# Kernel tuning notes

Hardware: AMD Instinct MI355X
Metric: run time of the kernel (lower is better)

## Reference

```python
import jax, jax.numpy as jnp
import numpy as np

ND, NA, E, EL, H, F = 100000, 50000, 500000, 200000, 128, 128


def setup_inputs() -> dict:
    key = jax.random.key(0)
    ks = jax.random.split(key, 20)
    def W(k, shape):
        return jax.random.normal(k, shape, dtype=jnp.float32) * 0.05
    inp = {
        'doc_x': jax.random.normal(ks[0], (ND, F), dtype=jnp.float32),
        'author_node_id': jnp.arange(NA, dtype=jnp.int64 if jax.config.jax_enable_x64 else jnp.int32),
        'edge_index': jnp.stack([
            jax.random.randint(ks[1], (E,), 0, ND),   # doc src
            jax.random.randint(ks[2], (E,), 0, NA),   # author dst
        ]),
        'edge_label_index': jnp.stack([
            jax.random.randint(ks[3], (EL,), 0, ND),
            jax.random.randint(ks[4], (EL,), 0, NA),
        ]),
        'doc_lin_W': W(ks[5], (F, H)), 'doc_lin_b': W(ks[6], (H,)),
        'author_emb': W(ks[7], (NA, H)),
        'c1_da_Wl': W(ks[8], (H, H)), 'c1_da_bl': W(ks[9], (H,)), 'c1_da_Wr': W(ks[10], (H, H)),
        'c1_ad_Wl': W(ks[11], (H, H)), 'c1_ad_bl': W(ks[12], (H,)), 'c1_ad_Wr': W(ks[13], (H, H)),
        'c2_da_Wl': W(ks[14], (H, H)), 'c2_da_bl': W(ks[15], (H,)), 'c2_da_Wr': W(ks[16], (H, H)),
        'c2_ad_Wl': W(ks[17], (H, H)), 'c2_ad_bl': W(ks[18], (H,)), 'c2_ad_Wr': W(ks[19], (H, H)),
    }
    return inp


def sage(x_src, x_dst, src, dst, num_dst, Wl, bl, Wr):
    # PyG SAGEConv (aggr='mean'): lin_l(mean_j x_src[j]) + lin_r(x_dst)
    msg = x_src[src]                                            # [E, H]
    agg = jax.ops.segment_sum(msg, dst, num_segments=num_dst)   # [num_dst, H]
    deg = jax.ops.segment_sum(jnp.ones_like(dst, dtype=x_src.dtype), dst, num_segments=num_dst)
    agg = agg / jnp.maximum(deg, 1.0)[:, None]
    return agg @ Wl + bl + x_dst @ Wr


def reference(doc_x, author_node_id, edge_index, edge_label_index,
              doc_lin_W, doc_lin_b, author_emb,
              c1_da_Wl, c1_da_bl, c1_da_Wr, c1_ad_Wl, c1_ad_bl, c1_ad_Wr,
              c2_da_Wl, c2_da_bl, c2_da_Wr, c2_ad_Wl, c2_ad_bl, c2_ad_Wr):
    x_doc = doc_x @ doc_lin_W + doc_lin_b          # [ND, H]
    x_author = author_emb[author_node_id]          # [NA, H]
    src_d, dst_a = edge_index[0], edge_index[1]
    # layer 1 (per-edge-type convs, to_hetero semantics) + ReLU
    h_a = sage(x_doc, x_author, src_d, dst_a, NA, c1_da_Wl, c1_da_bl, c1_da_Wr)
    h_d = sage(x_author, x_doc, dst_a, src_d, ND, c1_ad_Wl, c1_ad_bl, c1_ad_Wr)
    h_a, h_d = jax.nn.relu(h_a), jax.nn.relu(h_d)
    # layer 2
    o_a = sage(h_d, h_a, src_d, dst_a, NA, c2_da_Wl, c2_da_bl, c2_da_Wr)
    o_d = sage(h_a, h_d, dst_a, src_d, ND, c2_ad_Wl, c2_ad_bl, c2_ad_Wr)
    # edge scorer: dot product of gathered endpoint embeddings
    pred = (o_d[edge_label_index[0]] * o_a[edge_label_index[1]]).sum(-1)  # [EL]
    return pred
```

## Files before the change

### kernel.cpp

```cpp
#include <hip/hip_runtime.h>

typedef unsigned short u16;
typedef __attribute__((ext_vector_type(8))) short vbf16x8;
typedef __attribute__((ext_vector_type(4))) float vf32x4;

__device__ __forceinline__ float bf2f(u16 u) {
    union { unsigned int i; float f; } v; v.i = ((unsigned int)u) << 16; return v.f;
}
__device__ __forceinline__ u16 f2bf(float f) {
    union { float f; unsigned int i; } v; v.f = f;
    return (u16)((v.i + 0x7fffu + ((v.i >> 16) & 1u)) >> 16);
}

struct TPack { const float* src[9]; u16* dst[9]; };

#define NBUK 256
#define NBLK_BIN 256
#define SCAP 24
#define OVFCAP 32768
#define PACK_SH 17

__global__ __launch_bounds__(256) void mega_prep_bin(
    TPack p, const float* __restrict__ emb, const int* __restrict__ ids,
    u16* __restrict__ xauth, int NA,
    const int* __restrict__ src, const int* __restrict__ dst,
    unsigned* __restrict__ stageD, unsigned* __restrict__ stageA,
    int* __restrict__ cntD, int* __restrict__ cntA,
    uint2* __restrict__ ovfD, uint2* __restrict__ ovfA, int* __restrict__ ovfn,
    int E, int shD, int shA, int prepB) {
    int b = blockIdx.x;
    if (b >= prepB) {
        __shared__ int lcnt[NBUK];
        int bb = b - prepB;
        const bool isD = bb < NBLK_BIN;
        const int blk = isD ? bb : bb - NBLK_BIN;
        const int* key = isD ? src : dst;
        const int* val = isD ? dst : src;
        const int shift = isD ? shD : shA;
        unsigned* stage = isD ? stageD : stageA;
        int* cnt = isD ? cntD : cntA;
        uint2* ovf = isD ? ovfD : ovfA;
        int* on = ovfn + (isD ? 0 : 1);
        const int per = (E + NBLK_BIN - 1) / NBLK_BIN;
        const int beg = blk * per;
        const int end = min(beg + per, E);
        for (int i = threadIdx.x; i < NBUK; i += 256) lcnt[i] = 0;
        __syncthreads();
        for (int e = beg + (int)threadIdx.x; e < end; e += 256) {
            int k = key[e], v = val[e];
            int bkt = k >> shift;
            int slot = atomicAdd(&lcnt[bkt], 1);
            if (slot < SCAP) {
                unsigned local = (unsigned)(k - (bkt << shift));
                stage[((size_t)bkt * NBLK_BIN + blk) * SCAP + slot] =
                    (local << PACK_SH) | (unsigned)v;
            } else {
                int oi = atomicAdd(on, 1);
                if (oi < OVFCAP) ovf[oi] = make_uint2((unsigned)k, (unsigned)v);
            }
        }
        __syncthreads();
        for (int i = threadIdx.x; i < NBUK; i += 256)
            cnt[(size_t)i * NBLK_BIN + blk] = min(lcnt[i], SCAP);
        return;
    }
    if (b < 576) {
        int mat = b / 64;
        const float* s = p.src[mat];
        u16* d = p.dst[mat];
        int i = (b % 64) * 256 + threadIdx.x;
        int k = i >> 7, n = i & 127;
        d[(size_t)n * 128 + k] = f2bf(s[(size_t)k * 128 + n]);
    } else {
        int gid = (b - 576) * 256 + threadIdx.x;
        if (gid >= NA * 16) return;
        int n = gid >> 4, f = gid & 15;
        int id = ids[n];
        const float* s = emb + (size_t)id * 128 + f * 8;
        float4 lo = *(const float4*)(s);
        float4 hi = *(const float4*)(s + 4);
        u16 o[8] = {f2bf(lo.x), f2bf(lo.y), f2bf(lo.z), f2bf(lo.w),
                    f2bf(hi.x), f2bf(hi.y), f2bf(hi.z), f2bf(hi.w)};
        *(uint4*)(xauth + (size_t)n * 128 + f * 8) = *(const uint4*)o;
    }
}

__global__ __launch_bounds__(256) void bucket_count(
    const unsigned* __restrict__ stageD, const unsigned* __restrict__ stageA,
    const int* __restrict__ cntD, const int* __restrict__ cntA,
    const uint2* __restrict__ ovfD, const uint2* __restrict__ ovfA,
    const int* __restrict__ ovfn,
    int* __restrict__ cnt_d, int* __restrict__ cnt_a,
    int ND, int NA, int shD, int shA) {
    __shared__ int hist[1024];
    __shared__ int segc[NBLK_BIN];
    const bool isD = (int)blockIdx.x < NBUK;
    const int b = isD ? (int)blockIdx.x : (int)blockIdx.x - NBUK;
    const int sh = isD ? shD : shA;
    const int N = isD ? ND : NA;
    const int base = b << sh;
    const int range = min(1 << sh, N - base);
    if (range <= 0) return;
    const unsigned* stage = (isD ? stageD : stageA) + (size_t)b * NBLK_BIN * SCAP;
    const int* scnt = (isD ? cntD : cntA) + (size_t)b * NBLK_BIN;
    const uint2* ovf = isD ? ovfD : ovfA;
    const int nov = min(ovfn[isD ? 0 : 1], OVFCAP);
    int* out = isD ? cnt_d : cnt_a;
    const int tid = threadIdx.x;
    for (int i = tid; i < (1 << sh); i += 256) hist[i] = 0;
    segc[tid] = scnt[tid];
    __syncthreads();
    for (int j = tid; j < NBLK_BIN * SCAP; j += 256) {
        int seg = j / SCAP, slot = j - seg * SCAP;
        if (slot < segc[seg])
            atomicAdd(&hist[stage[j] >> PACK_SH], 1);
    }
    for (int i = tid; i < nov; i += 256) {
        int k = (int)ovf[i].x;
        if ((k >> sh) == b) atomicAdd(&hist[k - base], 1);
    }
    __syncthreads();
    for (int i = tid; i < range; i += 256) out[base + i] = hist[i];
}

__global__ __launch_bounds__(256) void scan1b(
    const int* __restrict__ cnt, int* __restrict__ incl,
    int* __restrict__ bs, int ND, int NA, int NBD) {
    __shared__ int sh[256];
    int b = blockIdx.x, tid = threadIdx.x;
    const int* in; int* out; int N; int lb;
    if (b < NBD) { in = cnt;      out = incl;      N = ND; lb = b; }
    else         { in = cnt + ND; out = incl + ND; N = NA; lb = b - NBD; }
    int gid = lb * 256 + tid;
    int v = gid < N ? in[gid] : 0;
    sh[tid] = v; __syncthreads();
    for (int off = 1; off < 256; off <<= 1) {
        int t = tid >= off ? sh[tid - off] : 0; __syncthreads();
        sh[tid] += t; __syncthreads();
    }
    if (gid < N) out[gid] = sh[tid];
    if (tid == 255) bs[b] = sh[255];
}

__global__ __launch_bounds__(256) void scan2b(int* __restrict__ bs, int NBD, int NBA) {
    __shared__ int sh[256];
    __shared__ int carry;
    int tid = threadIdx.x;
    for (int seg = 0; seg < 2; ++seg) {
        int* p = seg ? bs + NBD : bs;
        int nb = seg ? NBA : NBD;
        if (tid == 0) carry = 0;
        __syncthreads();
        for (int base = 0; base < nb; base += 256) {
            int i = base + tid;
            int v = i < nb ? p[i] : 0;
            sh[tid] = v; __syncthreads();
            for (int off = 1; off < 256; off <<= 1) {
                int t = tid >= off ? sh[tid - off] : 0; __syncthreads();
                sh[tid] += t; __syncthreads();
            }
            if (i < nb) p[i] = carry + sh[tid] - v;
            __syncthreads();
            if (tid == 255) carry += sh[255];
            __syncthreads();
        }
    }
}

__global__ __launch_bounds__(256) void scan3b(
    const int* __restrict__ incl, const int* __restrict__ bs,
    int* __restrict__ offs_d, int* __restrict__ offs_a,
    int ND, int NA, int NBD) {
    int b = blockIdx.x, tid = threadIdx.x;
    if (b < NBD) {
        int gid = b * 256 + tid;
        if (gid < ND) offs_d[gid + 1] = incl[gid] + bs[b];
        if (gid == 0) offs_d[0] = 0;
    } else {
        int gid = (b - NBD) * 256 + tid;
        if (gid < NA) offs_a[gid + 1] = incl[ND + gid] + bs[b];
        if (gid == 0) offs_a[0] = 0;
    }
}

__global__ __launch_bounds__(256) void bucket_fill2(
    const unsigned* __restrict__ stageD, const unsigned* __restrict__ stageA,
    const int* __restrict__ cntD, const int* __restrict__ cntA,
    const uint2* __restrict__ ovfD, const uint2* __restrict__ ovfA,
    const int* __restrict__ ovfn,
    const int* __restrict__ offs_d, const int* __restrict__ offs_a,
    int* __restrict__ nbr_d, int* __restrict__ nbr_a,
    int ND, int NA, int shD, int shA) {
    __shared__ int lcur[1024];
    __shared__ int segc[NBLK_BIN];
    const bool isD = (int)blockIdx.x < NBUK;
    const int b = isD ? (int)blockIdx.x : (int)blockIdx.x - NBUK;
    const int sh = isD ? shD : shA;
    const int N = isD ? ND : NA;
    const int base = b << sh;
    const int range = min(1 << sh, N - base);
    if (range <= 0) return;
    const unsigned* stage = (isD ? stageD : stageA) + (size_t)b * NBLK_BIN * SCAP;
    const int* scnt = (isD ? cntD : cntA) + (size_t)b * NBLK_BIN;
    const uint2* ovf = isD ? ovfD : ovfA;
    const int nov = min(ovfn[isD ? 0 : 1], OVFCAP);
    const int* offs = isD ? offs_d : offs_a;
    int* nbr = isD ? nbr_d : nbr_a;
    const int tid = threadIdx.x;
    for (int i = tid; i < range; i += 256) lcur[i] = offs[base + i];
    segc[tid] = scnt[tid];
    __syncthreads();
    for (int j = tid; j < NBLK_BIN * SCAP; j += 256) {
        int seg = j / SCAP, slot = j - seg * SCAP;
        if (slot < segc[seg]) {
            unsigned pk = stage[j];
            int local = pk >> PACK_SH;
            int v = (int)(pk & ((1u << PACK_SH) - 1u));
            nbr[atomicAdd(&lcur[local], 1)] = v;
        }
    }
    for (int i = tid; i < nov; i += 256) {
        int k = (int)ovf[i].x;
        if ((k >> sh) == b)
            nbr[atomicAdd(&lcur[k - base], 1)] = (int)ovf[i].y;
    }
}

__global__ __launch_bounds__(256) void agg_mean2(
    const u16* __restrict__ xa, const int* __restrict__ offs_a,
    const int* __restrict__ nbr_a, u16* __restrict__ outa, int NA,
    const u16* __restrict__ xd, const int* __restrict__ offs_d,
    const int* __restrict__ nbr_d, u16* __restrict__ outd, int ND) {
    int gid = blockIdx.x * 256 + threadIdx.x;
    int node = gid >> 4, f = gid & 15;
    int lane = threadIdx.x & 63;
    int gbase = lane & 48;
    const u16* x; const int* offs; const int* nbr; u16* out;
    if (node < NA) { x = xa; offs = offs_a; nbr = nbr_a; out = outa; }
    else {
        node -= NA;
        if (node >= ND) return;
        x = xd; offs = offs_d; nbr = nbr_d; out = outd;
    }
    int beg = offs[node], end = offs[node + 1];
    float acc[8] = {0, 0, 0, 0, 0, 0, 0, 0};

    for (int i = beg; i < end; i += 16) {
        int cnt = end - i; if (cnt > 16) cnt = 16;
        int myn = (i + f < end) ? nbr[i + f] : 0;
        int t = 0;
        for (; t + 3 < cnt; t += 4) {
            int i0 = __shfl(myn, gbase + t);
            int i1 = __shfl(myn, gbase + t + 1);
            int i2 = __shfl(myn, gbase + t + 2);
            int i3 = __shfl(myn, gbase + t + 3);
            uint4 q0 = *(const uint4*)(x + (size_t)i0 * 128 + f * 8);
            uint4 q1 = *(const uint4*)(x + (size_t)i1 * 128 + f * 8);
            uint4 q2 = *(const uint4*)(x + (size_t)i2 * 128 + f * 8);
            uint4 q3 = *(const uint4*)(x + (size_t)i3 * 128 + f * 8);
            acc[0] += bf2f((u16)(q0.x & 0xffff)) + bf2f((u16)(q1.x & 0xffff))
                    + bf2f((u16)(q2.x & 0xffff)) + bf2f((u16)(q3.x & 0xffff));
            acc[1] += bf2f((u16)(q0.x >> 16))    + bf2f((u16)(q1.x >> 16))
                    + bf2f((u16)(q2.x >> 16))    + bf2f((u16)(q3.x >> 16));
            acc[2] += bf2f((u16)(q0.y & 0xffff)) + bf2f((u16)(q1.y & 0xffff))
                    + bf2f((u16)(q2.y & 0xffff)) + bf2f((u16)(q3.y & 0xffff));
            acc[3] += bf2f((u16)(q0.y >> 16))    + bf2f((u16)(q1.y >> 16))
                    + bf2f((u16)(q2.y >> 16))    + bf2f((u16)(q3.y >> 16));
            acc[4] += bf2f((u16)(q0.z & 0xffff)) + bf2f((u16)(q1.z & 0xffff))
                    + bf2f((u16)(q2.z & 0xffff)) + bf2f((u16)(q3.z & 0xffff));
            acc[5] += bf2f((u16)(q0.z >> 16))    + bf2f((u16)(q1.z >> 16))
                    + bf2f((u16)(q2.z >> 16))    + bf2f((u16)(q3.z >> 16));
            acc[6] += bf2f((u16)(q0.w & 0xffff)) + bf2f((u16)(q1.w & 0xffff))
                    + bf2f((u16)(q2.w & 0xffff)) + bf2f((u16)(q3.w & 0xffff));
            acc[7] += bf2f((u16)(q0.w >> 16))    + bf2f((u16)(q1.w >> 16))
                    + bf2f((u16)(q2.w >> 16))    + bf2f((u16)(q3.w >> 16));
        }
        for (; t < cnt; ++t) {
            int i0 = __shfl(myn, gbase + t);
            uint4 q0 = *(const uint4*)(x + (size_t)i0 * 128 + f * 8);
            acc[0] += bf2f((u16)(q0.x & 0xffff));
            acc[1] += bf2f((u16)(q0.x >> 16));
            acc[2] += bf2f((u16)(q0.y & 0xffff));
            acc[3] += bf2f((u16)(q0.y >> 16));
            acc[4] += bf2f((u16)(q0.z & 0xffff));
            acc[5] += bf2f((u16)(q0.z >> 16));
            acc[6] += bf2f((u16)(q0.w & 0xffff));
            acc[7] += bf2f((u16)(q0.w >> 16));
        }
    }
    float inv = 1.0f / fmaxf((float)(end - beg), 1.0f);
    u16 o[8];
#pragma unroll
    for (int j = 0; j < 8; ++j) o[j] = f2bf(acc[j] * inv);
    *(uint4*)(out + (size_t)node * 128 + f * 8) = *(const uint4*)o;
}

__global__ __launch_bounds__(256) void doc_gemm(
    const float* __restrict__ A1f, const u16* __restrict__ W1T,
    const float* __restrict__ bias, u16* __restrict__ out, const int M) {
    __shared__ u16 WS[128 * 128];
    const int tid = threadIdx.x;
    const int lane = tid & 63, wave = tid >> 6;
    const int r15 = lane & 15, kq = lane >> 4;
    const int rowbase = blockIdx.x * 128 + wave * 32;
    const int m0 = rowbase + r15, m1 = rowbase + 16 + r15;
    const bool v0 = rowbase < M, v1 = rowbase + 16 < M;

    vf32x4 acc0[8], acc1[8];
#pragma unroll
    for (int i = 0; i < 8; ++i) { acc0[i] = (vf32x4)(0.0f); acc1[i] = (vf32x4)(0.0f); }

#pragma unroll
    for (int i = 0; i < 8; ++i) {
        int L = i * 256 + tid;
        int n = L >> 4, bk = L & 15;
        uint4 v = *(const uint4*)(W1T + (size_t)L * 8);
        *(uint4*)(WS + ((size_t)n * 16 + (bk ^ (n & 15))) * 8) = v;
    }
    __syncthreads();

#pragma unroll
    for (int ks = 0; ks < 4; ++ks) {
        vbf16x8 a0 = (vbf16x8)(short)0, a1 = (vbf16x8)(short)0;
        if (v0) {
            const float* p = A1f + (size_t)m0 * 128 + ks * 32 + kq * 8;
            float4 lo = *(const float4*)p, hi = *(const float4*)(p + 4);
            a0[0] = (short)f2bf(lo.x); a0[1] = (short)f2bf(lo.y);
            a0[2] = (short)f2bf(lo.z); a0[3] = (short)f2bf(lo.w);
            a0[4] = (short)f2bf(hi.x); a0[5] = (short)f2bf(hi.y);
            a0[6] = (short)f2bf(hi.z); a0[7] = (short)f2bf(hi.w);
        }
        if (v1) {
            const float* p = A1f + (size_t)m1 * 128 + ks * 32 + kq * 8;
            float4 lo = *(const float4*)p, hi = *(const float4*)(p + 4);
            a1[0] = (short)f2bf(lo.x); a1[1] = (short)f2bf(lo.y);
            a1[2] = (short)f2bf(lo.z); a1[3] = (short)f2bf(lo.w);
            a1[4] = (short)f2bf(hi.x); a1[5] = (short)f2bf(hi.y);
            a1[6] = (short)f2bf(hi.z); a1[7] = (short)f2bf(hi.w);
        }
#pragma unroll
        for (int nt = 0; nt < 8; ++nt) {
            vbf16x8 b = *(const vbf16x8*)(
                WS + ((size_t)(nt * 16 + r15) * 16 + ((ks * 4 + kq) ^ r15)) * 8);
            acc0[nt] = __builtin_amdgcn_mfma_f32_16x16x32_bf16(a0, b, acc0[nt], 0, 0, 0);
            acc1[nt] = __builtin_amdgcn_mfma_f32_16x16x32_bf16(a1, b, acc1[nt], 0, 0, 0);
        }
    }

#pragma unroll
    for (int nt = 0; nt < 8; ++nt) {
        const float bv = bias[nt * 16 + r15];
#pragma unroll
        for (int r = 0; r < 4; ++r) {
            if (v0) out[(size_t)(rowbase + kq * 4 + r) * 128 + nt * 16 + r15] =
                f2bf(acc0[nt][r] + bv);
            if (v1) out[(size_t)(rowbase + 16 + kq * 4 + r) * 128 + nt * 16 + r15] =
                f2bf(acc1[nt][r] + bv);
        }
    }
}

struct SideParams {
    const u16* A1b; const u16* W1T;
    const u16* A2b; const u16* W2T;
    const float* bias; u16* out;
    int M; int do_relu; int nblocks;
};
__global__ __launch_bounds__(256) void conv_gemm2(SideParams sa, SideParams sd) {
    __shared__ u16 WS[128 * 128];
    const bool isA = (int)blockIdx.x < sa.nblocks;
    SideParams P = isA ? sa : sd;
    const int bx = isA ? blockIdx.x : blockIdx.x - sa.nblocks;
    const int tid = threadIdx.x;
    const int lane = tid & 63, wave = tid >> 6;
    const int r15 = lane & 15, kq = lane >> 4;
    const int rowbase = bx * 128 + wave * 32;
    const int m0 = rowbase + r15, m1 = rowbase + 16 + r15;
    const bool v0 = rowbase < P.M, v1 = rowbase + 16 < P.M;

    vf32x4 acc0[8], acc1[8];
#pragma unroll
    for (int i = 0; i < 8; ++i) { acc0[i] = (vf32x4)(0.0f); acc1[i] = (vf32x4)(0.0f); }

#pragma unroll
    for (int mat = 0; mat < 2; ++mat) {
        const u16* WT = mat ? P.W2T : P.W1T;
        if (mat) __syncthreads();
#pragma unroll
        for (int i = 0; i < 8; ++i) {
            int L = i * 256 + tid;
            int n = L >> 4, bk = L & 15;
            uint4 v = *(const uint4*)(WT + (size_t)L * 8);
            *(uint4*)(WS + ((size_t)n * 16 + (bk ^ (n & 15))) * 8) = v;
        }
        __syncthreads();

        const u16* Ab = mat ? P.A2b : P.A1b;
#pragma unroll
        for (int ks = 0; ks < 4; ++ks) {
            vbf16x8 a0 = (vbf16x8)(short)0, a1 = (vbf16x8)(short)0;
            if (v0) a0 = *(const vbf16x8*)(Ab + (size_t)m0 * 128 + ks * 32 + kq * 8);
            if (v1) a1 = *(const vbf16x8*)(Ab + (size_t)m1 * 128 + ks * 32 + kq * 8);
#pragma unroll
            for (int nt = 0; nt < 8; ++nt) {
                vbf16x8 b = *(const vbf16x8*)(
                    WS + ((size_t)(nt * 16 + r15) * 16 + ((ks * 4 + kq) ^ r15)) * 8);
                acc0[nt] = __builtin_amdgcn_mfma_f32_16x16x32_bf16(a0, b, acc0[nt], 0, 0, 0);
                acc1[nt] = __builtin_amdgcn_mfma_f32_16x16x32_bf16(a1, b, acc1[nt], 0, 0, 0);
            }
        }
    }

#pragma unroll
    for (int nt = 0; nt < 8; ++nt) {
        const float bv = P.bias[nt * 16 + r15];
#pragma unroll
        for (int r = 0; r < 4; ++r) {
            if (v0) {
                float v = acc0[nt][r] + bv;
                if (P.do_relu) v = fmaxf(v, 0.0f);
                P.out[(size_t)(rowbase + kq * 4 + r) * 128 + nt * 16 + r15] = f2bf(v);
            }
            if (v1) {
                float v = acc1[nt][r] + bv;
                if (P.do_relu) v = fmaxf(v, 0.0f);
                P.out[(size_t)(rowbase + 16 + kq * 4 + r) * 128 + nt * 16 + r15] = f2bf(v);
            }
        }
    }
}

__global__ __launch_bounds__(256) void edge_dot(
    const u16* __restrict__ od, const u16* __restrict__ oa,
    const int* __restrict__ i0, const int* __restrict__ i1,
    float* __restrict__ pred, int EL) {
    int gid = blockIdx.x * 256 + threadIdx.x;
    if (gid >= EL * 16) return;
    int e = gid >> 4, f = gid & 15;
    uint4 x = *(const uint4*)(od + (size_t)i0[e] * 128 + f * 8);
    uint4 y = *(const uint4*)(oa + (size_t)i1[e] * 128 + f * 8);
    float s = 0.0f;
    s += bf2f((u16)(x.x & 0xffff)) * bf2f((u16)(y.x & 0xffff));
    s += bf2f((u16)(x.x >> 16))    * bf2f((u16)(y.x >> 16));
    s += bf2f((u16)(x.y & 0xffff)) * bf2f((u16)(y.y & 0xffff));
    s += bf2f((u16)(x.y >> 16))    * bf2f((u16)(y.y >> 16));
    s += bf2f((u16)(x.z & 0xffff)) * bf2f((u16)(y.z & 0xffff));
    s += bf2f((u16)(x.z >> 16))    * bf2f((u16)(y.z >> 16));
    s += bf2f((u16)(x.w & 0xffff)) * bf2f((u16)(y.w & 0xffff));
    s += bf2f((u16)(x.w >> 16))    * bf2f((u16)(y.w >> 16));
    s += __shfl_xor(s, 1);
    s += __shfl_xor(s, 2);
    s += __shfl_xor(s, 4);
    s += __shfl_xor(s, 8);
    if (f == 0) pred[e] = s;
}

extern "C" void kernel_launch(void* const* d_in, const int* in_sizes, int n_in,
                              void* d_out, int out_size, void* d_ws, size_t ws_size,
                              hipStream_t stream) {
    const float* doc_x    = (const float*)d_in[0];
    const int*   auth_id  = (const int*)d_in[1];
    const int*   eidx     = (const int*)d_in[2];
    const int*   elidx    = (const int*)d_in[3];
    const float* W_doc    = (const float*)d_in[4];
    const float* b_doc    = (const float*)d_in[5];
    const float* emb      = (const float*)d_in[6];
    const float* c1_da_Wl = (const float*)d_in[7];
    const float* c1_da_bl = (const float*)d_in[8];
    const float* c1_da_Wr = (const float*)d_in[9];
    const float* c1_ad_Wl = (const float*)d_in[10];
    const float* c1_ad_bl = (const float*)d_in[11];
    const float* c1_ad_Wr = (const float*)d_in[12];
    const float* c2_da_Wl = (const float*)d_in[13];
    const float* c2_da_bl = (const float*)d_in[14];
    const float* c2_da_Wr = (const float*)d_in[15];
    const float* c2_ad_Wl = (const float*)d_in[16];
    const float* c2_ad_bl = (const float*)d_in[17];
    const float* c2_ad_Wr = (const float*)d_in[18];

    const int ND = in_sizes[0] / 128;
    const int NA = in_sizes[1];
    const int E  = in_sizes[2] / 2;
    const int EL = in_sizes[3] / 2;
    const int* e_src = eidx;
    const int* e_dst = eidx + E;
    const int NBD = (ND + 255) / 256, NBA = (NA + 255) / 256;
    const int BA = (NA + 127) / 128, BD = (ND + 127) / 128;
    const int prepB = 576 + (NA * 16 + 255) / 256;

    char* base = (char*)d_ws;
    size_t off = 0;
    auto alloc = [&](size_t bytes) {
        void* p = base + off;
        off = (off + bytes + 255) & ~(size_t)255;
        return p;
    };
    u16*  xdoc  = (u16*)alloc((size_t)ND * 128 * 2);
    u16*  xauth = (u16*)alloc((size_t)NA * 128 * 2);
    u16*  hd    = (u16*)alloc((size_t)ND * 128 * 2);
    u16*  ha    = (u16*)alloc((size_t)NA * 128 * 2);
    u16*  aggA  = (u16*)alloc((size_t)NA * 128 * 2);
    u16*  aggD  = (u16*)alloc((size_t)ND * 128 * 2);
    u16*  wt    = (u16*)alloc((size_t)9 * 128 * 128 * 2);
    int*  cnt   = (int*)alloc((size_t)(ND + NA) * 4);
    int*  incl  = (int*)alloc((size_t)(ND + NA) * 4);
    int*  bs    = (int*)alloc((size_t)(NBD + NBA) * 4);
    int*  offs_d = (int*)alloc((size_t)(ND + 1) * 4);
    int*  offs_a = (int*)alloc((size_t)(NA + 1) * 4);
    int*  nbr_d = (int*)alloc((size_t)E * 4);
    int*  nbr_a = (int*)alloc((size_t)E * 4);
    int*  cntD  = (int*)alloc((size_t)NBUK * NBLK_BIN * 4);
    int*  cntA  = (int*)alloc((size_t)NBUK * NBLK_BIN * 4);
    uint2* ovfD = (uint2*)alloc((size_t)OVFCAP * 8);
    uint2* ovfA = (uint2*)alloc((size_t)OVFCAP * 8);
    int*  ovfn  = (int*)alloc(256);
    (void)ws_size; (void)n_in; (void)out_size;
    u16* od = xdoc;
    u16* oa = xauth;
    unsigned* stageD = (unsigned*)aggD;
    unsigned* stageA = (unsigned*)aggA;

    TPack tp;
    const float* srcs[9] = {W_doc, c1_da_Wl, c1_da_Wr, c1_ad_Wl, c1_ad_Wr,
                            c2_da_Wl, c2_da_Wr, c2_ad_Wl, c2_ad_Wr};
    for (int i = 0; i < 9; ++i) { tp.src[i] = srcs[i]; tp.dst[i] = wt + (size_t)i * 16384; }
    const u16 *WTdoc = wt, *WT_c1daL = wt + 16384, *WT_c1daR = wt + 2 * 16384,
              *WT_c1adL = wt + 3 * 16384, *WT_c1adR = wt + 4 * 16384,
              *WT_c2daL = wt + 5 * 16384, *WT_c2daR = wt + 6 * 16384,
              *WT_c2adL = wt + 7 * 16384, *WT_c2adR = wt + 8 * 16384;

    int shD = 0; while (((ND - 1) >> shD) >= NBUK) ++shD;
    int shA = 0; while (((NA - 1) >> shA) >= NBUK) ++shA;

    hipMemsetAsync(ovfn, 0, 8, stream);
    mega_prep_bin<<<prepB + 2 * NBLK_BIN, 256, 0, stream>>>(
        tp, emb, auth_id, xauth, NA, e_src, e_dst,
        stageD, stageA, cntD, cntA, ovfD, ovfA, ovfn, E, shD, shA, prepB);

    bucket_count<<<2 * NBUK, 256, 0, stream>>>(
        stageD, stageA, cntD, cntA, ovfD, ovfA, ovfn, cnt, cnt + ND,
        ND, NA, shD, shA);

    scan1b<<<NBD + NBA, 256, 0, stream>>>(cnt, incl, bs, ND, NA, NBD);
    scan2b<<<1, 256, 0, stream>>>(bs, NBD, NBA);
    scan3b<<<NBD + NBA, 256, 0, stream>>>(incl, bs, offs_d, offs_a, ND, NA, NBD);

    bucket_fill2<<<2 * NBUK, 256, 0, stream>>>(
        stageD, stageA, cntD, cntA, ovfD, ovfA, ovfn, offs_d, offs_a,
        nbr_d, nbr_a, ND, NA, shD, shA);

    doc_gemm<<<BD, 256, 0, stream>>>(doc_x, WTdoc, b_doc, xdoc, ND);

    const int aggGrid = ((NA + ND) * 16 + 255) / 256;

    agg_mean2<<<aggGrid, 256, 0, stream>>>(
        xdoc, offs_a, nbr_a, aggA, NA, xauth, offs_d, nbr_d, aggD, ND);
    {
        SideParams sa = {aggA, WT_c1daL, xauth, WT_c1daR, c1_da_bl, ha, NA, 1, BA};
        SideParams sd = {aggD, WT_c1adL, xdoc,  WT_c1adR, c1_ad_bl, hd, ND, 1, BD};
        conv_gemm2<<<BA + BD, 256, 0, stream>>>(sa, sd);
    }

    agg_mean2<<<aggGrid, 256, 0, stream>>>(
        hd, offs_a, nbr_a, aggA, NA, ha, offs_d, nbr_d, aggD, ND);
    {
        SideParams sa = {aggA, WT_c2daL, ha, WT_c2daR, c2_da_bl, oa, NA, 0, BA};
        SideParams sd = {aggD, WT_c2adL, hd, WT_c2adR, c2_ad_bl, od, ND, 0, BD};
        conv_gemm2<<<BA + BD, 256, 0, stream>>>(sa, sd);
    }

    edge_dot<<<(EL * 16 + 255) / 256, 256, 0, stream>>>(
        od, oa, elidx, elidx + EL, (float*)d_out, EL);
}
```

Before: 390.0 us.

## Make dense GEMMs persistent with weight reuse and register prefetch of next tile

Result: faster. 372.1 us (-4.6%).

```diff
diff --git a/kernel.cpp b/kernel.cpp
--- a/kernel.cpp
+++ b/kernel.cpp
@@ -295,112 +295,66 @@
     *(uint4*)(out + (size_t)node * 128 + f * 8) = *(const uint4*)o;
 }
 
-__global__ __launch_bounds__(256) void doc_gemm(
+__global__ __launch_bounds__(256) void doc_gemm3(
     const float* __restrict__ A1f, const u16* __restrict__ W1T,
-    const float* __restrict__ bias, u16* __restrict__ out, const int M) {
+    const float* __restrict__ bias, u16* __restrict__ out,
+    const int M, const int ntiles, const int gblocks) {
     __shared__ u16 WS[128 * 128];
     const int tid = threadIdx.x;
     const int lane = tid & 63, wave = tid >> 6;
     const int r15 = lane & 15, kq = lane >> 4;
-    const int rowbase = blockIdx.x * 128 + wave * 32;
-    const int m0 = rowbase + r15, m1 = rowbase + 16 + r15;
-    const bool v0 = rowbase < M, v1 = rowbase + 16 < M;
-
-    vf32x4 acc0[8], acc1[8];
-#pragma unroll
-    for (int i = 0; i < 8; ++i) { acc0[i] = (vf32x4)(0.0f); acc1[i] = (vf32x4)(0.0f); }
+    const int gb = blockIdx.x;
 
 #pragma unroll
     for (int i = 0; i < 8; ++i) {
         int L = i * 256 + tid;
         int n = L >> 4, bk = L & 15;
-        uint4 v = *(const uint4*)(W1T + (size_t)L * 8);
-        *(uint4*)(WS + ((size_t)n * 16 + (bk ^ (n & 15))) * 8) = v;
+        *(uint4*)(WS + ((size_t)n * 16 + (bk ^ (n & 15))) * 8) =
+            *(const uint4*)(W1T + (size_t)L * 8);
     }
     __syncthreads();
-
-#pragma unroll
-    for (int ks = 0; ks < 4; ++ks) {
-        vbf16x8 a0 = (vbf16x8)(short)0, a1 = (vbf16x8)(short)0;
-        if (v0) {
-            const float* p = A1f + (size_t)m0 * 128 + ks * 32 + kq * 8;
-            float4 lo = *(const float4*)p, hi = *(const float4*)(p + 4);
-            a0[0] = (short)f2bf(lo.x); a0[1] = (short)f2bf(lo.y);
-            a0[2] = (short)f2bf(lo.z); a0[3] = (short)f2bf(lo.w);
-            a0[4] = (short)f2bf(hi.x); a0[5] = (short)f2bf(hi.y);
-            a0[6] = (short)f2bf(hi.z); a0[7] = (short)f2bf(hi.w);
-        }
-        if (v1) {
-            const float* p = A1f + (size_t)m1 * 128 + ks * 32 + kq * 8;
-            float4 lo = *(const float4*)p, hi = *(const float4*)(p + 4);
-            a1[0] = (short)f2bf(lo.x); a1[1] = (short)f2bf(lo.y);
-            a1[2] = (short)f2bf(lo.z); a1[3] = (short)f2bf(lo.w);
-            a1[4] = (short)f2bf(hi.x); a1[5] = (short)f2bf(hi.y);
-            a1[6] = (short)f2bf(hi.z); a1[7] = (short)f2bf(hi.w);
-        }
-#pragma unroll
-        for (int nt = 0; nt < 8; ++nt) {
-            vbf16x8 b = *(const vbf16x8*)(
-                WS + ((size_t)(nt * 16 + r15) * 16 + ((ks * 4 + kq) ^ r15)) * 8);
-            acc0[nt] = __builtin_amdgcn_mfma_f32_16x16x32_bf16(a0, b, acc0[nt], 0, 0, 0);
-            acc1[nt] = __builtin_amdgcn_mfma_f32_16x16x32_bf16(a1, b, acc1[nt], 0, 0, 0);
-        }
-    }
-
-#pragma unroll
-    for (int nt = 0; nt < 8; ++nt) {
-        const float bv = bias[nt * 16 + r15];
-#pragma unroll
-        for (int r = 0; r < 4; ++r) {
-            if (v0) out[(size_t)(rowbase + kq * 4 + r) * 128 + nt * 16 + r15] =
-                f2bf(acc0[nt][r] + bv);
-            if (v1) out[(size_t)(rowbase + 16 + kq * 4 + r) * 128 + nt * 16 + r15] =
-                f2bf(acc1[nt][r] + bv);
-        }
-    }
-}
-
-struct SideParams {
-    const u16* A1b; const u16* W1T;
-    const u16* A2b; const u16* W2T;
-    const float* bias; u16* out;
-    int M; int do_relu; int nblocks;
-};
-__global__ __launch_bounds__(256) void conv_gemm2(SideParams sa, SideParams sd) {
-    __shared__ u16 WS[128 * 128];
-    const bool isA = (int)blockIdx.x < sa.nblocks;
-    SideParams P = isA ? sa : sd;
-    const int bx = isA ? blockIdx.x : blockIdx.x - sa.nblocks;
-    const int tid = threadIdx.x;
-    const int lane = tid & 63, wave = tid >> 6;
-    const int r15 = lane & 15, kq = lane >> 4;
-    const int rowbase = bx * 128 + wave * 32;
-    const int m0 = rowbase + r15, m1 = rowbase + 16 + r15;
-    const bool v0 = rowbase < P.M, v1 = rowbase + 16 < P.M;
-
-    vf32x4 acc0[8], acc1[8];
-#pragma unroll
-    for (int i = 0; i < 8; ++i) { acc0[i] = (vf32x4)(0.0f); acc1[i] = (vf32x4)(0.0f); }
-
-#pragma unroll
-    for (int mat = 0; mat < 2; ++mat) {
-        const u16* WT = mat ? P.W2T : P.W1T;
-        if (mat) __syncthreads();
-#pragma unroll
-        for (int i = 0; i < 8; ++i) {
-            int L = i * 256 + tid;
-            int n = L >> 4, bk = L & 15;
-            uint4 v = *(const uint4*)(WT + (size_t)L * 8);
-            *(uint4*)(WS + ((size_t)n * 16 + (bk ^ (n & 15))) * 8) = v;
-        }
-        __syncthreads();
-
-        const u16* Ab = mat ? P.A2b : P.A1b;
+    float bv[8];
+#pragma unroll
+    for (int nt = 0; nt < 8; ++nt) bv[nt] = bias[nt * 16 + r15];
+
+    auto loadraw = [&](int tile, float4* l0, float4* h0, float4* l1, float4* h1) {
+        const int rowbase = tile * 128 + wave * 32;
+        const int m0 = rowbase + r15, m1 = rowbase + 16 + r15;
+        const bool v0 = rowbase < M, v1 = rowbase + 16 < M;
+        const float4 z = {0.f, 0.f, 0.f, 0.f};
 #pragma unroll
         for (int ks = 0; ks < 4; ++ks) {
-            vbf16x8 a0 = (vbf16x8)(short)0, a1 = (vbf16x8)(short)0;
-            if (v0) a0 = *(const vbf16x8*)(Ab + (size_t)m0 * 128 + ks * 32 + kq * 8);
-            if (v1) a1 = *(const vbf16x8*)(Ab + (size_t)m1 * 128 + ks * 32 + kq * 8);
+            const float* p0 = A1f + (size_t)m0 * 128 + ks * 32 + kq * 8;
+            const float* p1 = A1f + (size_t)m1 * 128 + ks * 32 + kq * 8;
+            l0[ks] = v0 ? *(const float4*)p0 : z;
+            h0[ks] = v0 ? *(const float4*)(p0 + 4) : z;
+            l1[ks] = v1 ? *(const float4*)p1 : z;
+            h1[ks] = v1 ? *(const float4*)(p1 + 4) : z;
+        }
+    };
+    auto cvt = [&](float4 lo, float4 hi) {
+        vbf16x8 a;
+        a[0] = (short)f2bf(lo.x); a[1] = (short)f2bf(lo.y);
+        a[2] = (short)f2bf(lo.z); a[3] = (short)f2bf(lo.w);
+        a[4] = (short)f2bf(hi.x); a[5] = (short)f2bf(hi.y);
+        a[6] = (short)f2bf(hi.z); a[7] = (short)f2bf(hi.w);
+        return a;
+    };
+
+    float4 cl0[4], ch0[4], cl1[4], ch1[4];
+    float4 nl0[4], nh0[4], nl1[4], nh1[4];
+    if (gb < ntiles) loadraw(gb, cl0, ch0, cl1, ch1);
+    for (int t = gb; t < ntiles; t += gblocks) {
+        const int tn = t + gblocks;
+        if (tn < ntiles) loadraw(tn, nl0, nh0, nl1, nh1);
+
+        vf32x4 acc0[8], acc1[8];
+#pragma unroll
+        for (int i = 0; i < 8; ++i) { acc0[i] = (vf32x4)(0.0f); acc1[i] = (vf32x4)(0.0f); }
+#pragma unroll
+        for (int ks = 0; ks < 4; ++ks) {
+            vbf16x8 a0 = cvt(cl0[ks], ch0[ks]);
+            vbf16x8 a1 = cvt(cl1[ks], ch1[ks]);
 #pragma unroll
             for (int nt = 0; nt < 8; ++nt) {
                 vbf16x8 b = *(const vbf16x8*)(
@@ -409,24 +363,120 @@
                 acc1[nt] = __builtin_amdgcn_mfma_f32_16x16x32_bf16(a1, b, acc1[nt], 0, 0, 0);
             }
         }
-    }
-
-#pragma unroll
-    for (int nt = 0; nt < 8; ++nt) {
-        const float bv = P.bias[nt * 16 + r15];
-#pragma unroll
-        for (int r = 0; r < 4; ++r) {
-            if (v0) {
-                float v = acc0[nt][r] + bv;
-                if (P.do_relu) v = fmaxf(v, 0.0f);
-                P.out[(size_t)(rowbase + kq * 4 + r) * 128 + nt * 16 + r15] = f2bf(v);
+
+        const int rowbase = t * 128 + wave * 32;
+        const bool v0 = rowbase < M, v1 = rowbase + 16 < M;
+#pragma unroll
+        for (int nt = 0; nt < 8; ++nt) {
+#pragma unroll
+            for (int r = 0; r < 4; ++r) {
+                if (v0) out[(size_t)(rowbase + kq * 4 + r) * 128 + nt * 16 + r15] =
+                    f2bf(acc0[nt][r] + bv[nt]);
+                if (v1) out[(size_t)(rowbase + 16 + kq * 4 + r) * 128 + nt * 16 + r15] =
+                    f2bf(acc1[nt][r] + bv[nt]);
             }
-            if (v1) {
-                float v = acc1[nt][r] + bv;
-                if (P.do_relu) v = fmaxf(v, 0.0f);
-                P.out[(size_t)(rowbase + 16 + kq * 4 + r) * 128 + nt * 16 + r15] = f2bf(v);
+        }
+#pragma unroll
+        for (int ks = 0; ks < 4; ++ks) {
+            cl0[ks] = nl0[ks]; ch0[ks] = nh0[ks];
+            cl1[ks] = nl1[ks]; ch1[ks] = nh1[ks];
+        }
+    }
+}
+
+struct SideParams3 {
+    const u16* A1b; const u16* W1T;
+    const u16* A2b; const u16* W2T;
+    const float* bias; u16* out;
+    int M; int do_relu; int ntiles; int gblocks;
+};
+__global__ __launch_bounds__(256) void conv_gemm3(SideParams3 sa, SideParams3 sd) {
+    __shared__ u16 WS[2 * 128 * 128];
+    const bool isA = (int)blockIdx.x < sa.gblocks;
+    SideParams3 P = isA ? sa : sd;
+    const int gb = isA ? (int)blockIdx.x : (int)blockIdx.x - sa.gblocks;
+    const int tid = threadIdx.x;
+    const int lane = tid & 63, wave = tid >> 6;
+    const int r15 = lane & 15, kq = lane >> 4;
+
+#pragma unroll
+    for (int i = 0; i < 8; ++i) {
+        int L = i * 256 + tid;
+        int n = L >> 4, bk = L & 15;
+        *(uint4*)(WS + ((size_t)n * 16 + (bk ^ (n & 15))) * 8) =
+            *(const uint4*)(P.W1T + (size_t)L * 8);
+        *(uint4*)(WS + 16384 + ((size_t)n * 16 + (bk ^ (n & 15))) * 8) =
+            *(const uint4*)(P.W2T + (size_t)L * 8);
+    }
+    __syncthreads();
+    float bv[8];
+#pragma unroll
+    for (int nt = 0; nt < 8; ++nt) bv[nt] = P.bias[nt * 16 + r15];
+
+    auto loadA = [&](const u16* Ab, int tile, vbf16x8* fa, vbf16x8* fb) {
+        const int rowbase = tile * 128 + wave * 32;
+        const int m0 = rowbase + r15, m1 = rowbase + 16 + r15;
+        const bool v0 = rowbase < P.M, v1 = rowbase + 16 < P.M;
+#pragma unroll
+        for (int ks = 0; ks < 4; ++ks) {
+            fa[ks] = v0 ? *(const vbf16x8*)(Ab + (size_t)m0 * 128 + ks * 32 + kq * 8)
+                        : (vbf16x8)(short)0;
+            fb[ks] = v1 ? *(const vbf16x8*)(Ab + (size_t)m1 * 128 + ks * 32 + kq * 8)
+                        : (vbf16x8)(short)0;
+        }
+    };
+
+    vbf16x8 c1a[4], c1b[4], c2a[4], c2b[4], n1a[4], n1b[4];
+    if (gb < P.ntiles) loadA(P.A1b, gb, c1a, c1b);
+    for (int t = gb; t < P.ntiles; t += P.gblocks) {
+        loadA(P.A2b, t, c2a, c2b);
+        const int tn = t + P.gblocks;
+        if (tn < P.ntiles) loadA(P.A1b, tn, n1a, n1b);
+
+        vf32x4 acc0[8], acc1[8];
+#pragma unroll
+        for (int i = 0; i < 8; ++i) { acc0[i] = (vf32x4)(0.0f); acc1[i] = (vf32x4)(0.0f); }
+#pragma unroll
+        for (int ks = 0; ks < 4; ++ks) {
+#pragma unroll
+            for (int nt = 0; nt < 8; ++nt) {
+                vbf16x8 b = *(const vbf16x8*)(
+                    WS + ((size_t)(nt * 16 + r15) * 16 + ((ks * 4 + kq) ^ r15)) * 8);
+                acc0[nt] = __builtin_amdgcn_mfma_f32_16x16x32_bf16(c1a[ks], b, acc0[nt], 0, 0, 0);
+                acc1[nt] = __builtin_amdgcn_mfma_f32_16x16x32_bf16(c1b[ks], b, acc1[nt], 0, 0, 0);
             }
         }
+#pragma unroll
+        for (int ks = 0; ks < 4; ++ks) {
+#pragma unroll
+            for (int nt = 0; nt < 8; ++nt) {
+                vbf16x8 b = *(const vbf16x8*)(
+                    WS + 16384 + ((size_t)(nt * 16 + r15) * 16 + ((ks * 4 + kq) ^ r15)) * 8);
+                acc0[nt] = __builtin_amdgcn_mfma_f32_16x16x32_bf16(c2a[ks], b, acc0[nt], 0, 0, 0);
+                acc1[nt] = __builtin_amdgcn_mfma_f32_16x16x32_bf16(c2b[ks], b, acc1[nt], 0, 0, 0);
+            }
+        }
+
+        const int rowbase = t * 128 + wave * 32;
+        const bool v0 = rowbase < P.M, v1 = rowbase + 16 < P.M;
+#pragma unroll
+        for (int nt = 0; nt < 8; ++nt) {
+#pragma unroll
+            for (int r = 0; r < 4; ++r) {
+                if (v0) {
+                    float v = acc0[nt][r] + bv[nt];
+                    if (P.do_relu) v = fmaxf(v, 0.0f);
+                    P.out[(size_t)(rowbase + kq * 4 + r) * 128 + nt * 16 + r15] = f2bf(v);
+                }
+                if (v1) {
+                    float v = acc1[nt][r] + bv[nt];
+                    if (P.do_relu) v = fmaxf(v, 0.0f);
+                    P.out[(size_t)(rowbase + 16 + kq * 4 + r) * 128 + nt * 16 + r15] = f2bf(v);
+                }
+            }
+        }
+#pragma unroll
+        for (int ks = 0; ks < 4; ++ks) { c1a[ks] = n1a[ks]; c1b[ks] = n1b[ks]; }
     }
 }
 
@@ -549,24 +599,26 @@
         stageD, stageA, cntD, cntA, ovfD, ovfA, ovfn, offs_d, offs_a,
         nbr_d, nbr_a, ND, NA, shD, shA);
 
-    doc_gemm<<<BD, 256, 0, stream>>>(doc_x, WTdoc, b_doc, xdoc, ND);
+    doc_gemm3<<<512, 256, 0, stream>>>(doc_x, WTdoc, b_doc, xdoc, ND, BD, 512);
 
     const int aggGrid = ((NA + ND) * 16 + 255) / 256;
+    const int gA = (int)(((long)512 * BA) / (BA + BD));
+    const int gD = 512 - gA;
 
     agg_mean2<<<aggGrid, 256, 0, stream>>>(
         xdoc, offs_a, nbr_a, aggA, NA, xauth, offs_d, nbr_d, aggD, ND);
     {
-        SideParams sa = {aggA, WT_c1daL, xauth, WT_c1daR, c1_da_bl, ha, NA, 1, BA};
-        SideParams sd = {aggD, WT_c1adL, xdoc,  WT_c1adR, c1_ad_bl, hd, ND, 1, BD};
-        conv_gemm2<<<BA + BD, 256, 0, stream>>>(sa, sd);
+        SideParams3 sa = {aggA, WT_c1daL, xauth, WT_c1daR, c1_da_bl, ha, NA, 1, BA, gA};
+        SideParams3 sd = {aggD, WT_c1adL, xdoc,  WT_c1adR, c1_ad_bl, hd, ND, 1, BD, gD};
+        conv_gemm3<<<gA + gD, 256, 0, stream>>>(sa, sd);
     }
 
     agg_mean2<<<aggGrid, 256, 0, stream>>>(
         hd, offs_a, nbr_a, aggA, NA, ha, offs_d, nbr_d, aggD, ND);
     {
-        SideParams sa = {aggA, WT_c2daL, ha, WT_c2daR, c2_da_bl, oa, NA, 0, BA};
-        SideParams sd = {aggD, WT_c2adL, hd, WT_c2adR, c2_ad_bl, od, ND, 0, BD};
-        conv_gemm2<<<BA + BD, 256, 0, stream>>>(sa, sd);
+        SideParams3 sa = {aggA, WT_c2daL, ha, WT_c2daR, c2_da_bl, oa, NA, 0, BA, gA};
+        SideParams3 sd = {aggD, WT_c2adL, hd, WT_c2adR, c2_ad_bl, od, ND, 0, BD, gD};
+        conv_gemm3<<<gA + gD, 256, 0, stream>>>(sa, sd);
     }
 
     edge_dot<<<(EL * 16 + 255) / 256, 256, 0, stream>>>(
```
